# Kernel tuning notes

Hardware: AMD Instinct MI355X
Metric: run time of the kernel (lower is better)

The kernel has to match this reference:

```python
import jax, jax.numpy as jnp
import numpy as np

H = 64  # hidden_size
F = 32  # input_size
B, T = 4096, 256


def setup_inputs() -> dict:
    key = jax.random.key(0)
    ks = jax.random.split(key, 12)
    s = 1.0 / np.sqrt(H)  # torch LSTM init scale
    u = lambda k, shape: jax.random.uniform(k, shape, jnp.float32, -s, s)
    return {
        "x": jax.random.normal(ks[0], (B, T, F), jnp.float32),
        # layer 0 (input_size=F)
        "W_ih0": u(ks[1], (4 * H, F)),
        "W_hh0": u(ks[2], (4 * H, H)),
        "b_ih0": u(ks[3], (4 * H,)),
        "b_hh0": u(ks[4], (4 * H,)),
        # layer 1 (input_size=H)
        "W_ih1": u(ks[5], (4 * H, H)),
        "W_hh1": u(ks[6], (4 * H, H)),
        "b_ih1": u(ks[7], (4 * H,)),
        "b_hh1": u(ks[8], (4 * H,)),
        # linear head
        "W_out": u(ks[9], (1, H)),
        "b_out": u(ks[10], (1,)),
    }


def _lstm_layer(x, W_ih, W_hh, b_ih, b_hh):
    # x: [B, T, D] -> hidden sequence [B, T, H]; PyTorch gate order i,f,g,o.
    b = x.shape[0]
    h_dim = W_hh.shape[1]
    # precompute input contribution for all timesteps: [B, T, 4H]
    gx = jnp.einsum('btd,gd->btg', x, W_ih) + b_ih + b_hh

    def step(carry, g_t):
        h, c = carry
        g = g_t + h @ W_hh.T  # [B, 4H]
        i, f, gg, o = jnp.split(g, 4, axis=-1)
        c = jax.nn.sigmoid(f) * c + jax.nn.sigmoid(i) * jnp.tanh(gg)
        h = jax.nn.sigmoid(o) * jnp.tanh(c)
        return (h, c), h

    h0 = jnp.zeros((b, h_dim), x.dtype)
    (_, _), hs = jax.lax.scan(step, (h0, h0), jnp.swapaxes(gx, 0, 1))
    return jnp.swapaxes(hs, 0, 1)  # [B, T, H]


def reference(x, W_ih0, W_hh0, b_ih0, b_hh0, W_ih1, W_hh1, b_ih1, b_hh1, W_out, b_out):
    h = _lstm_layer(x, W_ih0, W_hh0, b_ih0, b_hh0)
    h = _lstm_layer(h, W_ih1, W_hh1, b_ih1, b_hh1)
    last = h[:, -1, :]  # [B, H]; dropout is identity at inference
    return last @ W_out.T + b_out  # [B, 1]
```

## Files before the change

### kernel.cpp

```cpp
#include <hip/hip_runtime.h>

typedef _Float16 half8 __attribute__((ext_vector_type(8)));
typedef _Float16 half4 __attribute__((ext_vector_type(4)));
typedef float f32x4 __attribute__((ext_vector_type(4)));

#define T_STEPS 256
#define NB      16
#define NBLOCKS (4096/NB)
#define LOG2E   1.4426950408889634f

#define SH 136

__device__ __forceinline__ half8 cvt8s(const float* __restrict__ p, float s) {
    half8 r;
    #pragma unroll
    for (int j = 0; j < 8; ++j) r[j] = (_Float16)(p[j] * s);
    return r;
}

__device__ __forceinline__ void sync_lds() {
    asm volatile("s_waitcnt lgkmcnt(0)" ::: "memory");
    __builtin_amdgcn_s_barrier();
}

__global__ __launch_bounds__(512, 1)
void lstm_v5(const float* __restrict__ x,
             const float* __restrict__ Wih0, const float* __restrict__ Whh0,
             const float* __restrict__ bih0, const float* __restrict__ bhh0,
             const float* __restrict__ Wih1, const float* __restrict__ Whh1,
             const float* __restrict__ bih1, const float* __restrict__ bhh1,
             const float* __restrict__ Wout, const float* __restrict__ bout,
             float* __restrict__ out)
{
    __shared__ _Float16 Hb[2][16][SH];

    const int tid  = threadIdx.x;
    const int w    = tid >> 6;
    const bool isL1 = (w < 4);
    const int wq   = w & 3;
    const int l    = tid & 63;
    const int ln   = l & 15;
    const int lb   = l >> 4;
    const int ub   = 16 * wq + 4 * lb;
    const int gb0  = blockIdx.x * NB;

    half8 wa[4][4];
    half8 wax[4];
    f32x4 bv[4];
    if (isL1) {
        #pragma unroll
        for (int q = 0; q < 4; ++q) {
            const float s = (q == 2) ? 2.f * LOG2E : -LOG2E;
            const int g = 64 * q + 16 * wq + ln;
            wax[q] = cvt8s(Wih0 + g * 32 + 8 * lb, s);
            #pragma unroll
            for (int ks = 0; ks < 2; ++ks)
                wa[q][ks] = cvt8s(Whh0 + g * 64 + 32 * ks + 8 * lb, s);
            #pragma unroll
            for (int jj = 0; jj < 4; ++jj) {
                const int gj = 64 * q + ub + jj;
                bv[q][jj] = (bih0[gj] + bhh0[gj]) * s;
            }
        }
    } else {
        #pragma unroll
        for (int q = 0; q < 4; ++q) {
            const float s = (q == 2) ? 2.f * LOG2E : -LOG2E;
            const int g = 64 * q + 16 * wq + ln;
            #pragma unroll
            for (int ks = 0; ks < 4; ++ks) {
                const int c0 = 32 * ks + 8 * lb;
                const float* p = (c0 < 64) ? (Wih1 + g * 64 + c0)
                                           : (Whh1 + g * 64 + (c0 - 64));
                wa[q][ks] = cvt8s(p, s);
            }
            #pragma unroll
            for (int jj = 0; jj < 4; ++jj) {
                const int gj = 64 * q + ub + jj;
                bv[q][jj] = (bih1[gj] + bhh1[gj]) * s;
            }
        }
    }

    float cst[4] = {0.f, 0.f, 0.f, 0.f};

    {
        unsigned int* z = (unsigned int*)Hb;
        for (int i = tid; i < (int)(sizeof(Hb) / 4); i += 512) z[i] = 0u;
    }

    const float* xb = x + (long)(gb0 + ln) * T_STEPS * 32 + 8 * lb;
    f32x4 xr0 = {0.f,0.f,0.f,0.f}, xr1 = {0.f,0.f,0.f,0.f};
    f32x4 gxA[4], gxB[4];
    if (isL1) {
        xr0 = *(const f32x4*)(xb);
        xr1 = *(const f32x4*)(xb + 4);
        half8 xf;
        #pragma unroll
        for (int j = 0; j < 4; ++j) { xf[j] = (_Float16)xr0[j]; xf[4+j] = (_Float16)xr1[j]; }
        #pragma unroll
        for (int q = 0; q < 4; ++q) {
            gxA[q] = bv[q];
            gxA[q] = __builtin_amdgcn_mfma_f32_16x16x32_f16(wax[q], xf, gxA[q], 0, 0, 0);
        }
        xr0 = *(const f32x4*)(xb + 32);
        xr1 = *(const f32x4*)(xb + 36);
    }
    sync_lds();

#define ACT1(A, JJ)                                                            \
    {                                                                          \
        const float ei = __builtin_amdgcn_exp2f(A[0][JJ]);                     \
        const float ef = __builtin_amdgcn_exp2f(A[1][JJ]);                     \
        const float Eg = __builtin_amdgcn_exp2f(A[2][JJ]);                     \
        const float eo = __builtin_amdgcn_exp2f(A[3][JJ]);                     \
        const float ti = 1.f + ei, tf = 1.f + ef, tg = 1.f + Eg;               \
        const float pig = ti * tg;                                             \
        const float num = fmaf(Eg - 1.f, tf, cst[JJ] * pig);                   \
        const float c   = num * __builtin_amdgcn_rcpf(pig * tf);               \
        cst[JJ] = c;                                                           \
        const float Ec  = __builtin_amdgcn_exp2f(fminf((2.f * LOG2E) * c, 120.f)); \
        hh[JJ] = (_Float16)((Ec - 1.f) *                                       \
                 __builtin_amdgcn_rcpf((1.f + eo) * (1.f + Ec)));              \
    }

#define STEP(J, P, GXC, GXN)                                                   \
    do {                                                                       \
        if (isL1 && (J) < T_STEPS) {                                           \
                                                \
            const half8 bf0 = *(const half8*)&Hb[P][ln][8 * lb];               \
            const half8 bf1 = *(const half8*)&Hb[P][ln][32 + 8 * lb];          \
                         \
            half8 xf;                                                          \
            _Pragma("unroll")                                                  \
            for (int j = 0; j < 4; ++j) { xf[j] = (_Float16)xr0[j]; xf[4+j] = (_Float16)xr1[j]; } \
            _Pragma("unroll")                                                  \
            for (int q = 0; q < 4; ++q) GXN[q] = bv[q];                        \
            _Pragma("unroll")                                                  \
            for (int q = 0; q < 4; ++q)                                        \
                GXN[q] = __builtin_amdgcn_mfma_f32_16x16x32_f16(wax[q], xf, GXN[q], 0, 0, 0); \
                          \
            { const int jn = ((J) + 2 < T_STEPS) ? (J) + 2 : T_STEPS - 1;      \
              xr0 = *(const f32x4*)(xb + jn * 32);                             \
              xr1 = *(const f32x4*)(xb + jn * 32 + 4); }                       \
                                                   \
            __builtin_amdgcn_s_setprio(1);                                     \
            _Pragma("unroll")                                                  \
            for (int q = 0; q < 4; ++q) {                                      \
                GXC[q] = __builtin_amdgcn_mfma_f32_16x16x32_f16(wa[q][0], bf0, GXC[q], 0, 0, 0); \
                GXC[q] = __builtin_amdgcn_mfma_f32_16x16x32_f16(wa[q][1], bf1, GXC[q], 0, 0, 0); \
            }                                                                  \
            __builtin_amdgcn_s_setprio(0);                                     \
            half4 hh;                                                          \
            ACT1(GXC, 0) ACT1(GXC, 1) ACT1(GXC, 2) ACT1(GXC, 3)                \
            *(half4*)&Hb[1 - (P)][ln][ub] = hh;                                \
        }                                                                      \
        if (!isL1 && (J) > 0) {                                                \
            const half8 bf0 = *(const half8*)&Hb[P][ln][8 * lb];               \
            const half8 bf1 = *(const half8*)&Hb[P][ln][32 + 8 * lb];          \
            const half8 bf2 = *(const half8*)&Hb[P][ln][64 + 8 * lb];          \
            const half8 bf3 = *(const half8*)&Hb[P][ln][96 + 8 * lb];          \
            f32x4 acc[4];                                                      \
            _Pragma("unroll")                                                  \
            for (int q = 0; q < 4; ++q) acc[q] = bv[q];                        \
            __builtin_amdgcn_s_setprio(1);                                     \
            _Pragma("unroll")                                                  \
            for (int q = 0; q < 4; ++q) {                                      \
                acc[q] = __builtin_amdgcn_mfma_f32_16x16x32_f16(wa[q][0], bf0, acc[q], 0, 0, 0); \
                acc[q] = __builtin_amdgcn_mfma_f32_16x16x32_f16(wa[q][1], bf1, acc[q], 0, 0, 0); \
                acc[q] = __builtin_amdgcn_mfma_f32_16x16x32_f16(wa[q][2], bf2, acc[q], 0, 0, 0); \
                acc[q] = __builtin_amdgcn_mfma_f32_16x16x32_f16(wa[q][3], bf3, acc[q], 0, 0, 0); \
            }                                                                  \
            __builtin_amdgcn_s_setprio(0);                                     \
            half4 hh;                                                          \
            ACT1(acc, 0) ACT1(acc, 1) ACT1(acc, 2) ACT1(acc, 3)                \
            *(half4*)&Hb[1 - (P)][ln][64 + ub] = hh;                           \
        }                                                                      \
        sync_lds();                                                            \
    } while (0)

    for (int jj = 0; jj < T_STEPS; jj += 2) {
        STEP(jj, 0, gxA, gxB);
        STEP(jj + 1, 1, gxB, gxA);
    }
    STEP(T_STEPS, 0, gxA, gxB);

    if (tid < NB) {
        float s = bout[0];
        #pragma unroll
        for (int u8 = 0; u8 < 8; ++u8) {
            const half8 hv = *(const half8*)&Hb[1][tid][64 + 8 * u8];
            #pragma unroll
            for (int j = 0; j < 8; ++j)
                s += (float)hv[j] * Wout[8 * u8 + j];
        }
        out[gb0 + tid] = s;
    }
}

extern "C" void kernel_launch(void* const* d_in, const int* in_sizes, int n_in,
                              void* d_out, int out_size, void* d_ws, size_t ws_size,
                              hipStream_t stream) {
    const float* x    = (const float*)d_in[0];
    const float* Wih0 = (const float*)d_in[1];
    const float* Whh0 = (const float*)d_in[2];
    const float* bih0 = (const float*)d_in[3];
    const float* bhh0 = (const float*)d_in[4];
    const float* Wih1 = (const float*)d_in[5];
    const float* Whh1 = (const float*)d_in[6];
    const float* bih1 = (const float*)d_in[7];
    const float* bhh1 = (const float*)d_in[8];
    const float* Wout = (const float*)d_in[9];
    const float* bout = (const float*)d_in[10];

    hipLaunchKernelGGL(lstm_v5, dim3(NBLOCKS), dim3(512), 0, stream,
                       x, Wih0, Whh0, bih0, bhh0,
                       Wih1, Whh1, bih1, bhh1, Wout, bout,
                       (float*)d_out);
}
```

Before: 174.2 us.

## Skew layer-2 pipeline by an extra step and prefetch layer-1 hidden state into registers

Layer-2 waves now trail layer 1 by two steps. They read the layer-1 hidden half one step early into registers (pf0/pf1), so the input-projection MFMAs can start from registers while only the recurrent half is read from LDS that step. The x prefetch is deepened to three steps ahead, the s_setprio calls are removed, and the Wih0 register array is folded into wa to save registers. The loop gains one extra iteration pair and the final hidden state is read from the other buffer, which adds latency at the tail.

```diff
diff --git a/kernel.cpp b/kernel.cpp
--- a/kernel.cpp
+++ b/kernel.cpp
@@ -24,13 +24,13 @@
 }
 
 __global__ __launch_bounds__(512, 1)
-void lstm_v5(const float* __restrict__ x,
-             const float* __restrict__ Wih0, const float* __restrict__ Whh0,
-             const float* __restrict__ bih0, const float* __restrict__ bhh0,
-             const float* __restrict__ Wih1, const float* __restrict__ Whh1,
-             const float* __restrict__ bih1, const float* __restrict__ bhh1,
-             const float* __restrict__ Wout, const float* __restrict__ bout,
-             float* __restrict__ out)
+void lstm_v10(const float* __restrict__ x,
+              const float* __restrict__ Wih0, const float* __restrict__ Whh0,
+              const float* __restrict__ bih0, const float* __restrict__ bhh0,
+              const float* __restrict__ Wih1, const float* __restrict__ Whh1,
+              const float* __restrict__ bih1, const float* __restrict__ bhh1,
+              const float* __restrict__ Wout, const float* __restrict__ bout,
+              float* __restrict__ out)
 {
     __shared__ _Float16 Hb[2][16][SH];
 
@@ -45,17 +45,16 @@
     const int gb0  = blockIdx.x * NB;
 
     half8 wa[4][4];
-    half8 wax[4];
     f32x4 bv[4];
     if (isL1) {
         #pragma unroll
         for (int q = 0; q < 4; ++q) {
             const float s = (q == 2) ? 2.f * LOG2E : -LOG2E;
             const int g = 64 * q + 16 * wq + ln;
-            wax[q] = cvt8s(Wih0 + g * 32 + 8 * lb, s);
+            wa[q][0] = cvt8s(Wih0 + g * 32 + 8 * lb, s);
             #pragma unroll
             for (int ks = 0; ks < 2; ++ks)
-                wa[q][ks] = cvt8s(Whh0 + g * 64 + 32 * ks + 8 * lb, s);
+                wa[q][1 + ks] = cvt8s(Whh0 + g * 64 + 32 * ks + 8 * lb, s);
             #pragma unroll
             for (int jj = 0; jj < 4; ++jj) {
                 const int gj = 64 * q + ub + jj;
@@ -91,21 +90,23 @@
 
     const float* xb = x + (long)(gb0 + ln) * T_STEPS * 32 + 8 * lb;
     f32x4 xr0 = {0.f,0.f,0.f,0.f}, xr1 = {0.f,0.f,0.f,0.f};
+    f32x4 xq0 = {0.f,0.f,0.f,0.f}, xq1 = {0.f,0.f,0.f,0.f};
     f32x4 gxA[4], gxB[4];
     if (isL1) {
-        xr0 = *(const f32x4*)(xb);
-        xr1 = *(const f32x4*)(xb + 4);
+        const f32x4 x0a = *(const f32x4*)(xb);
+        const f32x4 x0b = *(const f32x4*)(xb + 4);
         half8 xf;
         #pragma unroll
-        for (int j = 0; j < 4; ++j) { xf[j] = (_Float16)xr0[j]; xf[4+j] = (_Float16)xr1[j]; }
-        #pragma unroll
-        for (int q = 0; q < 4; ++q) {
-            gxA[q] = bv[q];
-            gxA[q] = __builtin_amdgcn_mfma_f32_16x16x32_f16(wax[q], xf, gxA[q], 0, 0, 0);
-        }
+        for (int j = 0; j < 4; ++j) { xf[j] = (_Float16)x0a[j]; xf[4+j] = (_Float16)x0b[j]; }
+        #pragma unroll
+        for (int q = 0; q < 4; ++q)
+            gxA[q] = __builtin_amdgcn_mfma_f32_16x16x32_f16(wa[q][0], xf, bv[q], 0, 0, 0);
         xr0 = *(const f32x4*)(xb + 32);
         xr1 = *(const f32x4*)(xb + 36);
-    }
+        xq0 = *(const f32x4*)(xb + 64);
+        xq1 = *(const f32x4*)(xb + 68);
+    }
+    half8 pf0 = {}, pf1 = {};
     sync_lds();
 
 #define ACT1(A, JJ)                                                            \
@@ -130,66 +131,68 @@
                                                 \
             const half8 bf0 = *(const half8*)&Hb[P][ln][8 * lb];               \
             const half8 bf1 = *(const half8*)&Hb[P][ln][32 + 8 * lb];          \
-                         \
+                           \
             half8 xf;                                                          \
             _Pragma("unroll")                                                  \
             for (int j = 0; j < 4; ++j) { xf[j] = (_Float16)xr0[j]; xf[4+j] = (_Float16)xr1[j]; } \
             _Pragma("unroll")                                                  \
-            for (int q = 0; q < 4; ++q) GXN[q] = bv[q];                        \
-            _Pragma("unroll")                                                  \
             for (int q = 0; q < 4; ++q)                                        \
-                GXN[q] = __builtin_amdgcn_mfma_f32_16x16x32_f16(wax[q], xf, GXN[q], 0, 0, 0); \
-                          \
-            { const int jn = ((J) + 2 < T_STEPS) ? (J) + 2 : T_STEPS - 1;      \
-              xr0 = *(const f32x4*)(xb + jn * 32);                             \
-              xr1 = *(const f32x4*)(xb + jn * 32 + 4); }                       \
-                                                   \
-            __builtin_amdgcn_s_setprio(1);                                     \
+                GXN[q] = __builtin_amdgcn_mfma_f32_16x16x32_f16(wa[q][0], xf, bv[q], 0, 0, 0); \
+                \
+            xr0 = xq0; xr1 = xq1;                                              \
+            { const int jn = ((J) + 3 < T_STEPS) ? (J) + 3 : T_STEPS - 1;      \
+              xq0 = *(const f32x4*)(xb + jn * 32);                             \
+              xq1 = *(const f32x4*)(xb + jn * 32 + 4); }                       \
+                                                           \
             _Pragma("unroll")                                                  \
             for (int q = 0; q < 4; ++q) {                                      \
-                GXC[q] = __builtin_amdgcn_mfma_f32_16x16x32_f16(wa[q][0], bf0, GXC[q], 0, 0, 0); \
-                GXC[q] = __builtin_amdgcn_mfma_f32_16x16x32_f16(wa[q][1], bf1, GXC[q], 0, 0, 0); \
+                GXC[q] = __builtin_amdgcn_mfma_f32_16x16x32_f16(wa[q][1], bf0, GXC[q], 0, 0, 0); \
+                GXC[q] = __builtin_amdgcn_mfma_f32_16x16x32_f16(wa[q][2], bf1, GXC[q], 0, 0, 0); \
             }                                                                  \
-            __builtin_amdgcn_s_setprio(0);                                     \
             half4 hh;                                                          \
             ACT1(GXC, 0) ACT1(GXC, 1) ACT1(GXC, 2) ACT1(GXC, 3)                \
             *(half4*)&Hb[1 - (P)][ln][ub] = hh;                                \
         }                                                                      \
-        if (!isL1 && (J) > 0) {                                                \
-            const half8 bf0 = *(const half8*)&Hb[P][ln][8 * lb];               \
-            const half8 bf1 = *(const half8*)&Hb[P][ln][32 + 8 * lb];          \
-            const half8 bf2 = *(const half8*)&Hb[P][ln][64 + 8 * lb];          \
-            const half8 bf3 = *(const half8*)&Hb[P][ln][96 + 8 * lb];          \
-            f32x4 acc[4];                                                      \
-            _Pragma("unroll")                                                  \
-            for (int q = 0; q < 4; ++q) acc[q] = bv[q];                        \
-            __builtin_amdgcn_s_setprio(1);                                     \
-            _Pragma("unroll")                                                  \
-            for (int q = 0; q < 4; ++q) {                                      \
-                acc[q] = __builtin_amdgcn_mfma_f32_16x16x32_f16(wa[q][0], bf0, acc[q], 0, 0, 0); \
-                acc[q] = __builtin_amdgcn_mfma_f32_16x16x32_f16(wa[q][1], bf1, acc[q], 0, 0, 0); \
-                acc[q] = __builtin_amdgcn_mfma_f32_16x16x32_f16(wa[q][2], bf2, acc[q], 0, 0, 0); \
-                acc[q] = __builtin_amdgcn_mfma_f32_16x16x32_f16(wa[q][3], bf3, acc[q], 0, 0, 0); \
+        if (!isL1) {                                                           \
+            if ((J) >= 2) {                                                    \
+                  \
+                const half8 bf2 = *(const half8*)&Hb[P][ln][64 + 8 * lb];      \
+                const half8 bf3 = *(const half8*)&Hb[P][ln][96 + 8 * lb];      \
+                f32x4 acc[4];                                                  \
+                _Pragma("unroll")                                              \
+                for (int q = 0; q < 4; ++q) {                                  \
+                    acc[q] = __builtin_amdgcn_mfma_f32_16x16x32_f16(wa[q][0], pf0, bv[q], 0, 0, 0); \
+                    acc[q] = __builtin_amdgcn_mfma_f32_16x16x32_f16(wa[q][1], pf1, acc[q], 0, 0, 0); \
+                }                                                              \
+                _Pragma("unroll")                                              \
+                for (int q = 0; q < 4; ++q) {                                  \
+                    acc[q] = __builtin_amdgcn_mfma_f32_16x16x32_f16(wa[q][2], bf2, acc[q], 0, 0, 0); \
+                    acc[q] = __builtin_amdgcn_mfma_f32_16x16x32_f16(wa[q][3], bf3, acc[q], 0, 0, 0); \
+                }                                                              \
+                   \
+                pf0 = *(const half8*)&Hb[P][ln][8 * lb];                       \
+                pf1 = *(const half8*)&Hb[P][ln][32 + 8 * lb];                  \
+                half4 hh;                                                      \
+                ACT1(acc, 0) ACT1(acc, 1) ACT1(acc, 2) ACT1(acc, 3)            \
+                *(half4*)&Hb[1 - (P)][ln][64 + ub] = hh;                       \
+            } else {                                                           \
+                pf0 = *(const half8*)&Hb[P][ln][8 * lb];                       \
+                pf1 = *(const half8*)&Hb[P][ln][32 + 8 * lb];                  \
             }                                                                  \
-            __builtin_amdgcn_s_setprio(0);                                     \
-            half4 hh;                                                          \
-            ACT1(acc, 0) ACT1(acc, 1) ACT1(acc, 2) ACT1(acc, 3)                \
-            *(half4*)&Hb[1 - (P)][ln][64 + ub] = hh;                           \
         }                                                                      \
         sync_lds();                                                            \
     } while (0)
 
-    for (int jj = 0; jj < T_STEPS; jj += 2) {
+    for (int jj = 0; jj < T_STEPS + 2; jj += 2) {
         STEP(jj, 0, gxA, gxB);
         STEP(jj + 1, 1, gxB, gxA);
     }
-    STEP(T_STEPS, 0, gxA, gxB);
 
     if (tid < NB) {
         float s = bout[0];
         #pragma unroll
         for (int u8 = 0; u8 < 8; ++u8) {
-            const half8 hv = *(const half8*)&Hb[1][tid][64 + 8 * u8];
+            const half8 hv = *(const half8*)&Hb[0][tid][64 + 8 * u8];
             #pragma unroll
             for (int j = 0; j < 8; ++j)
                 s += (float)hv[j] * Wout[8 * u8 + j];
@@ -213,7 +216,7 @@
     const float* Wout = (const float*)d_in[9];
     const float* bout = (const float*)d_in[10];
 
-    hipLaunchKernelGGL(lstm_v5, dim3(NBLOCKS), dim3(512), 0, stream,
+    hipLaunchKernelGGL(lstm_v10, dim3(NBLOCKS), dim3(512), 0, stream,
                        x, Wih0, Whh0, bih0, bhh0,
                        Wih1, Whh1, bih1, bhh1, Wout, bout,
                        (float*)d_out);
```

Measured after the change: 185.6 us. 1.07x slower.

## Split LSTM gates across 16 waves with interleaved gate rows per lane

Applied to the files above, without the earlier changes.

Doubles the block to 1024 threads, with 8 waves per layer instead of 4. Each wave now handles 8 hidden units, and the weight rows are permuted so one MFMA output column holds all four gates (i,f,g,o) of a single unit. That halves the MFMA count and the activation work per wave on the serial recurrence path and drops the per-step bias copies. The cost is scalar half stores to LDS in place of half4 vector stores, more waves sharing each barrier, and a launch-bounds change to (1024,4) that may constrain register allocation.

```diff
diff --git a/kernel.cpp b/kernel.cpp
--- a/kernel.cpp
+++ b/kernel.cpp
@@ -1,7 +1,6 @@
 #include <hip/hip_runtime.h>
 
 typedef _Float16 half8 __attribute__((ext_vector_type(8)));
-typedef _Float16 half4 __attribute__((ext_vector_type(4)));
 typedef float f32x4 __attribute__((ext_vector_type(4)));
 
 #define T_STEPS 256
@@ -23,158 +22,150 @@
     __builtin_amdgcn_s_barrier();
 }
 
-__global__ __launch_bounds__(512, 1)
-void lstm_v5(const float* __restrict__ x,
-             const float* __restrict__ Wih0, const float* __restrict__ Whh0,
-             const float* __restrict__ bih0, const float* __restrict__ bhh0,
-             const float* __restrict__ Wih1, const float* __restrict__ Whh1,
-             const float* __restrict__ bih1, const float* __restrict__ bhh1,
-             const float* __restrict__ Wout, const float* __restrict__ bout,
-             float* __restrict__ out)
+__global__ __launch_bounds__(1024, 4)
+void lstm_v12(const float* __restrict__ x,
+              const float* __restrict__ Wih0, const float* __restrict__ Whh0,
+              const float* __restrict__ bih0, const float* __restrict__ bhh0,
+              const float* __restrict__ Wih1, const float* __restrict__ Whh1,
+              const float* __restrict__ bih1, const float* __restrict__ bhh1,
+              const float* __restrict__ Wout, const float* __restrict__ bout,
+              float* __restrict__ out)
 {
     __shared__ _Float16 Hb[2][16][SH];
 
     const int tid  = threadIdx.x;
     const int w    = tid >> 6;
-    const bool isL1 = (w < 4);
-    const int wq   = w & 3;
+    const bool isL1 = (w < 8);
+    const int wq   = w & 7;
     const int l    = tid & 63;
     const int ln   = l & 15;
     const int lb   = l >> 4;
-    const int ub   = 16 * wq + 4 * lb;
+    const int U0   = 8 * wq;
     const int gb0  = blockIdx.x * NB;
 
-    half8 wa[4][4];
-    half8 wax[4];
-    f32x4 bv[4];
+    const int qa = ln & 3;
+    const int ua = ln >> 2;
+    const float sa = (qa == 2) ? 2.f * LOG2E : -LOG2E;
+
+    half8 wa[2][4];
+    f32x4 bv[2];
     if (isL1) {
         #pragma unroll
-        for (int q = 0; q < 4; ++q) {
-            const float s = (q == 2) ? 2.f * LOG2E : -LOG2E;
-            const int g = 64 * q + 16 * wq + ln;
-            wax[q] = cvt8s(Wih0 + g * 32 + 8 * lb, s);
-            #pragma unroll
-            for (int ks = 0; ks < 2; ++ks)
-                wa[q][ks] = cvt8s(Whh0 + g * 64 + 32 * ks + 8 * lb, s);
+        for (int t = 0; t < 2; ++t) {
+            const int gr = 64 * qa + U0 + 4 * t + ua;
+            wa[t][0] = cvt8s(Wih0 + gr * 32 + 8 * lb, sa);
+            wa[t][1] = cvt8s(Whh0 + gr * 64 + 8 * lb, sa);
+            wa[t][2] = cvt8s(Whh0 + gr * 64 + 32 + 8 * lb, sa);
             #pragma unroll
             for (int jj = 0; jj < 4; ++jj) {
-                const int gj = 64 * q + ub + jj;
-                bv[q][jj] = (bih0[gj] + bhh0[gj]) * s;
+                const int g = 64 * jj + U0 + 4 * t + lb;
+                const float s = (jj == 2) ? 2.f * LOG2E : -LOG2E;
+                bv[t][jj] = (bih0[g] + bhh0[g]) * s;
             }
         }
     } else {
         #pragma unroll
-        for (int q = 0; q < 4; ++q) {
-            const float s = (q == 2) ? 2.f * LOG2E : -LOG2E;
-            const int g = 64 * q + 16 * wq + ln;
+        for (int t = 0; t < 2; ++t) {
+            const int gr = 64 * qa + U0 + 4 * t + ua;
             #pragma unroll
             for (int ks = 0; ks < 4; ++ks) {
                 const int c0 = 32 * ks + 8 * lb;
-                const float* p = (c0 < 64) ? (Wih1 + g * 64 + c0)
-                                           : (Whh1 + g * 64 + (c0 - 64));
-                wa[q][ks] = cvt8s(p, s);
+                const float* p = (c0 < 64) ? (Wih1 + gr * 64 + c0)
+                                           : (Whh1 + gr * 64 + (c0 - 64));
+                wa[t][ks] = cvt8s(p, sa);
             }
             #pragma unroll
             for (int jj = 0; jj < 4; ++jj) {
-                const int gj = 64 * q + ub + jj;
-                bv[q][jj] = (bih1[gj] + bhh1[gj]) * s;
+                const int g = 64 * jj + U0 + 4 * t + lb;
+                const float s = (jj == 2) ? 2.f * LOG2E : -LOG2E;
+                bv[t][jj] = (bih1[g] + bhh1[g]) * s;
             }
         }
     }
 
-    float cst[4] = {0.f, 0.f, 0.f, 0.f};
+    float cst0 = 0.f, cst1 = 0.f;
 
     {
         unsigned int* z = (unsigned int*)Hb;
-        for (int i = tid; i < (int)(sizeof(Hb) / 4); i += 512) z[i] = 0u;
+        for (int i = tid; i < (int)(sizeof(Hb) / 4); i += 1024) z[i] = 0u;
     }
 
     const float* xb = x + (long)(gb0 + ln) * T_STEPS * 32 + 8 * lb;
     f32x4 xr0 = {0.f,0.f,0.f,0.f}, xr1 = {0.f,0.f,0.f,0.f};
-    f32x4 gxA[4], gxB[4];
+    f32x4 gxA[2], gxB[2];
     if (isL1) {
-        xr0 = *(const f32x4*)(xb);
-        xr1 = *(const f32x4*)(xb + 4);
+        const f32x4 x0a = *(const f32x4*)(xb);
+        const f32x4 x0b = *(const f32x4*)(xb + 4);
         half8 xf;
         #pragma unroll
-        for (int j = 0; j < 4; ++j) { xf[j] = (_Float16)xr0[j]; xf[4+j] = (_Float16)xr1[j]; }
-        #pragma unroll
-        for (int q = 0; q < 4; ++q) {
-            gxA[q] = bv[q];
-            gxA[q] = __builtin_amdgcn_mfma_f32_16x16x32_f16(wax[q], xf, gxA[q], 0, 0, 0);
-        }
+        for (int j = 0; j < 4; ++j) { xf[j] = (_Float16)x0a[j]; xf[4+j] = (_Float16)x0b[j]; }
+        gxA[0] = __builtin_amdgcn_mfma_f32_16x16x32_f16(wa[0][0], xf, bv[0], 0, 0, 0);
+        gxA[1] = __builtin_amdgcn_mfma_f32_16x16x32_f16(wa[1][0], xf, bv[1], 0, 0, 0);
         xr0 = *(const f32x4*)(xb + 32);
         xr1 = *(const f32x4*)(xb + 36);
     }
     sync_lds();
 
-#define ACT1(A, JJ)                                                            \
+#define ACT_U(AV, CS, HOUT)                                                    \
     {                                                                          \
-        const float ei = __builtin_amdgcn_exp2f(A[0][JJ]);                     \
-        const float ef = __builtin_amdgcn_exp2f(A[1][JJ]);                     \
-        const float Eg = __builtin_amdgcn_exp2f(A[2][JJ]);                     \
-        const float eo = __builtin_amdgcn_exp2f(A[3][JJ]);                     \
+        const float ei = __builtin_amdgcn_exp2f(AV[0]);                        \
+        const float ef = __builtin_amdgcn_exp2f(AV[1]);                        \
+        const float Eg = __builtin_amdgcn_exp2f(AV[2]);                        \
+        const float eo = __builtin_amdgcn_exp2f(AV[3]);                        \
         const float ti = 1.f + ei, tf = 1.f + ef, tg = 1.f + Eg;               \
         const float pig = ti * tg;                                             \
-        const float num = fmaf(Eg - 1.f, tf, cst[JJ] * pig);                   \
+        const float num = fmaf(Eg - 1.f, tf, (CS) * pig);                      \
         const float c   = num * __builtin_amdgcn_rcpf(pig * tf);               \
-        cst[JJ] = c;                                                           \
+        (CS) = c;                                                              \
         const float Ec  = __builtin_amdgcn_exp2f(fminf((2.f * LOG2E) * c, 120.f)); \
-        hh[JJ] = (_Float16)((Ec - 1.f) *                                       \
-                 __builtin_amdgcn_rcpf((1.f + eo) * (1.f + Ec)));              \
+        HOUT = (_Float16)((Ec - 1.f) *                                         \
+               __builtin_amdgcn_rcpf((1.f + eo) * (1.f + Ec)));                \
     }
 
 #define STEP(J, P, GXC, GXN)                                                   \
     do {                                                                       \
         if (isL1 && (J) < T_STEPS) {                                           \
-                                                \
             const half8 bf0 = *(const half8*)&Hb[P][ln][8 * lb];               \
             const half8 bf1 = *(const half8*)&Hb[P][ln][32 + 8 * lb];          \
-                         \
             half8 xf;                                                          \
             _Pragma("unroll")                                                  \
             for (int j = 0; j < 4; ++j) { xf[j] = (_Float16)xr0[j]; xf[4+j] = (_Float16)xr1[j]; } \
-            _Pragma("unroll")                                                  \
-            for (int q = 0; q < 4; ++q) GXN[q] = bv[q];                        \
-            _Pragma("unroll")                                                  \
-            for (int q = 0; q < 4; ++q)                                        \
-                GXN[q] = __builtin_amdgcn_mfma_f32_16x16x32_f16(wax[q], xf, GXN[q], 0, 0, 0); \
-                          \
+            GXN[0] = __builtin_amdgcn_mfma_f32_16x16x32_f16(wa[0][0], xf, bv[0], 0, 0, 0); \
+            GXN[1] = __builtin_amdgcn_mfma_f32_16x16x32_f16(wa[1][0], xf, bv[1], 0, 0, 0); \
             { const int jn = ((J) + 2 < T_STEPS) ? (J) + 2 : T_STEPS - 1;      \
               xr0 = *(const f32x4*)(xb + jn * 32);                             \
               xr1 = *(const f32x4*)(xb + jn * 32 + 4); }                       \
-                                                   \
             __builtin_amdgcn_s_setprio(1);                                     \
-            _Pragma("unroll")                                                  \
-            for (int q = 0; q < 4; ++q) {                                      \
-                GXC[q] = __builtin_amdgcn_mfma_f32_16x16x32_f16(wa[q][0], bf0, GXC[q], 0, 0, 0); \
-                GXC[q] = __builtin_amdgcn_mfma_f32_16x16x32_f16(wa[q][1], bf1, GXC[q], 0, 0, 0); \
-            }                                                                  \
+            GXC[0] = __builtin_amdgcn_mfma_f32_16x16x32_f16(wa[0][1], bf0, GXC[0], 0, 0, 0); \
+            GXC[1] = __builtin_amdgcn_mfma_f32_16x16x32_f16(wa[1][1], bf0, GXC[1], 0, 0, 0); \
+            GXC[0] = __builtin_amdgcn_mfma_f32_16x16x32_f16(wa[0][2], bf1, GXC[0], 0, 0, 0); \
+            GXC[1] = __builtin_amdgcn_mfma_f32_16x16x32_f16(wa[1][2], bf1, GXC[1], 0, 0, 0); \
             __builtin_amdgcn_s_setprio(0);                                     \
-            half4 hh;                                                          \
-            ACT1(GXC, 0) ACT1(GXC, 1) ACT1(GXC, 2) ACT1(GXC, 3)                \
-            *(half4*)&Hb[1 - (P)][ln][ub] = hh;                                \
+            _Float16 h0v, h1v;                                                 \
+            ACT_U(GXC[0], cst0, h0v) ACT_U(GXC[1], cst1, h1v)                  \
+            Hb[1 - (P)][ln][U0 + lb]     = h0v;                                \
+            Hb[1 - (P)][ln][U0 + 4 + lb] = h1v;                                \
         }                                                                      \
-        if (!isL1 && (J) > 0) {                                                \
+        if (!isL1 && (J) >= 1 && (J) <= T_STEPS) {                             \
             const half8 bf0 = *(const half8*)&Hb[P][ln][8 * lb];               \
             const half8 bf1 = *(const half8*)&Hb[P][ln][32 + 8 * lb];          \
             const half8 bf2 = *(const half8*)&Hb[P][ln][64 + 8 * lb];          \
             const half8 bf3 = *(const half8*)&Hb[P][ln][96 + 8 * lb];          \
-            f32x4 acc[4];                                                      \
-            _Pragma("unroll")                                                  \
-            for (int q = 0; q < 4; ++q) acc[q] = bv[q];                        \
+            f32x4 a0 = bv[0], a1 = bv[1];                                      \
             __builtin_amdgcn_s_setprio(1);                                     \
-            _Pragma("unroll")                                                  \
-            for (int q = 0; q < 4; ++q) {                                      \
-                acc[q] = __builtin_amdgcn_mfma_f32_16x16x32_f16(wa[q][0], bf0, acc[q], 0, 0, 0); \
-                acc[q] = __builtin_amdgcn_mfma_f32_16x16x32_f16(wa[q][1], bf1, acc[q], 0, 0, 0); \
-                acc[q] = __builtin_amdgcn_mfma_f32_16x16x32_f16(wa[q][2], bf2, acc[q], 0, 0, 0); \
-                acc[q] = __builtin_amdgcn_mfma_f32_16x16x32_f16(wa[q][3], bf3, acc[q], 0, 0, 0); \
-            }                                                                  \
+            a0 = __builtin_amdgcn_mfma_f32_16x16x32_f16(wa[0][0], bf0, a0, 0, 0, 0); \
+            a1 = __builtin_amdgcn_mfma_f32_16x16x32_f16(wa[1][0], bf0, a1, 0, 0, 0); \
+            a0 = __builtin_amdgcn_mfma_f32_16x16x32_f16(wa[0][1], bf1, a0, 0, 0, 0); \
+            a1 = __builtin_amdgcn_mfma_f32_16x16x32_f16(wa[1][1], bf1, a1, 0, 0, 0); \
+            a0 = __builtin_amdgcn_mfma_f32_16x16x32_f16(wa[0][2], bf2, a0, 0, 0, 0); \
+            a1 = __builtin_amdgcn_mfma_f32_16x16x32_f16(wa[1][2], bf2, a1, 0, 0, 0); \
+            a0 = __builtin_amdgcn_mfma_f32_16x16x32_f16(wa[0][3], bf3, a0, 0, 0, 0); \
+            a1 = __builtin_amdgcn_mfma_f32_16x16x32_f16(wa[1][3], bf3, a1, 0, 0, 0); \
             __builtin_amdgcn_s_setprio(0);                                     \
-            half4 hh;                                                          \
-            ACT1(acc, 0) ACT1(acc, 1) ACT1(acc, 2) ACT1(acc, 3)                \
-            *(half4*)&Hb[1 - (P)][ln][64 + ub] = hh;                           \
+            _Float16 h0v, h1v;                                                 \
+            ACT_U(a0, cst0, h0v) ACT_U(a1, cst1, h1v)                          \
+            Hb[1 - (P)][ln][64 + U0 + lb]     = h0v;                           \
+            Hb[1 - (P)][ln][64 + U0 + 4 + lb] = h1v;                           \
         }                                                                      \
         sync_lds();                                                            \
     } while (0)
@@ -213,7 +204,7 @@
     const float* Wout = (const float*)d_in[9];
     const float* bout = (const float*)d_in[10];
 
-    hipLaunchKernelGGL(lstm_v5, dim3(NBLOCKS), dim3(512), 0, stream,
+    hipLaunchKernelGGL(lstm_v12, dim3(NBLOCKS), dim3(1024), 0, stream,
                        x, Wih0, Whh0, bih0, bhh0,
                        Wih1, Whh1, bih1, bhh1, Wout, bout,
                        (float*)d_out);
```

After: 181.1 us. 1.04x slower.
